# Kernel tuning notes

Hardware: AMD Instinct MI355X
Metric: run time of the kernel (lower is better)

Reference implementation:

```python
import jax, jax.numpy as jnp
import numpy as np

B, T, D = 64, 512, 1024

def setup_inputs() -> dict:
    key = jax.random.key(0)
    k1, k2, k3 = jax.random.split(key, 3)
    q1 = jax.random.normal(k1, (B, T, D), dtype=jnp.float32)
    q2 = jax.random.normal(k2, (B, T, D), dtype=jnp.float32)
    # original uses 'uniform' init; scale like a small uniform weight
    U = jax.random.uniform(k3, (D, D), dtype=jnp.float32, minval=-0.05, maxval=0.05)
    return {"q1": q1, "q2": q2, "U": U}

def reference(q1, q2, U):
    # bilinear scores: (q1 @ U) @ q2^T -> [B, T1, T2]
    att = jnp.einsum('btd,de,bse->bts', q1, U, q2)
    att = jax.nn.relu(att)
    w1_att = jax.nn.softmax(att, axis=1)  # softmax over q1 timesteps
    w2_att = jax.nn.softmax(att, axis=2)  # softmax over q2 timesteps
    # q1_align = w1_att^T @ q1 -> [B, T2, D]
    q1_align = jnp.einsum('bts,btd->bsd', w1_att, q1)
    # q2_align = w2_att @ q2 -> [B, T1, D]
    q2_align = jnp.einsum('bts,bsd->btd', w2_att, q2)
    return (q1_align, q2_align)
```

## Files before the change

kernel.cpp:

```cpp
#include <hip/hip_runtime.h>
#include <hip/hip_bf16.h>
#include <math.h>

#define B_DIM 64
#define T_DIM 512
#define D_DIM 1024
#define TT (T_DIM * T_DIM)
#define TD (T_DIM * D_DIM)
#define PSTR ((long)B_DIM * T_DIM)

typedef _Float16 f16;
typedef f16 f16x4 __attribute__((ext_vector_type(4)));
typedef f16 f16x8 __attribute__((ext_vector_type(8)));
typedef float f32x4 __attribute__((ext_vector_type(4)));

__device__ __forceinline__ void gld_lds16(const void* g, void* l) {
    __builtin_amdgcn_global_load_lds(
        (const __attribute__((address_space(1))) void*)g,
        (__attribute__((address_space(3))) void*)l, 16, 0, 0);
}

#define SWZ(r) (((r) >> 1) & 3)

template <int EPI>
__global__ __launch_bounds__(512, 2) void k_mfma2(
        const f16* __restrict__ A, int lda,
        const f16* __restrict__ Bt, int ldb, int K,
        void* __restrict__ Cout, int ldc,
        const float2* __restrict__ scaleP,
        long batchA, long batchB, long batchC,
        float2* __restrict__ rowP, float2* __restrict__ colP) {
    __shared__ __align__(16) f16 LA[2][8192];
    __shared__ __align__(16) f16 LB[2][8192];

    const int tid = threadIdx.x;
    const int lane = tid & 63, w = tid >> 6;

    const int gX = gridDim.x, gY = gridDim.y;
    int nwg = gX * gY * gridDim.z;
    int o = blockIdx.x + gX * (blockIdx.y + gY * blockIdx.z);
    int q8 = nwg >> 3;
    int fl = (o & 7) * q8 + (o >> 3);
    const int bx = fl % gX;
    int tmp = fl / gX;
    const int by = tmp % gY;
    const int bz = tmp / gY;

    const f16* Ab = A + (long)bz * batchA + (long)(by * 256) * lda;
    const f16* Bb = Bt + (long)bz * batchB + (long)(bx * 256) * ldb;

    const int r0 = tid >> 2, s0 = (tid & 3) ^ SWZ(r0);
    const int r1 = r0 + 128, s1 = (tid & 3) ^ SWZ(r1);
    const long offA0 = (long)r0 * lda + s0 * 8;
    const long offA1 = (long)r1 * lda + s1 * 8;
    const long offB0 = (long)r0 * ldb + s0 * 8;
    const long offB1 = (long)r1 * ldb + s1 * 8;
    const int ldsOff0 = w * 512;
    const int ldsOff1 = 4096 + w * 512;

    const int g = lane >> 4;
    const int rA0 = (w & 1) * 128 + (lane & 15);
    const int rB0 = (w >> 1) * 64 + (lane & 15);

    f32x4 acc[8][4] = {};

    gld_lds16(Ab + offA0, &LA[0][ldsOff0]);
    gld_lds16(Ab + offA1, &LA[0][ldsOff1]);
    gld_lds16(Bb + offB0, &LB[0][ldsOff0]);
    gld_lds16(Bb + offB1, &LB[0][ldsOff1]);
    __syncthreads();

    const int NT = K >> 5;
    for (int t = 0; t < NT; ++t) {
        const int cur = t & 1;
        if (t + 1 < NT) {
            const long kt = (long)(t + 1) << 5;
            gld_lds16(Ab + offA0 + kt, &LA[cur ^ 1][ldsOff0]);
            gld_lds16(Ab + offA1 + kt, &LA[cur ^ 1][ldsOff1]);
            gld_lds16(Bb + offB0 + kt, &LB[cur ^ 1][ldsOff0]);
            gld_lds16(Bb + offB1 + kt, &LB[cur ^ 1][ldsOff1]);
        }
        f16x8 a[8], b[4];
#pragma unroll
        for (int m = 0; m < 8; ++m) {
            int r = rA0 + m * 16;
            a[m] = *(const f16x8*)(&LA[cur][r * 32 + ((g ^ SWZ(r)) << 3)]);
        }
#pragma unroll
        for (int n = 0; n < 4; ++n) {
            int r = rB0 + n * 16;
            b[n] = *(const f16x8*)(&LB[cur][r * 32 + ((g ^ SWZ(r)) << 3)]);
        }
        __builtin_amdgcn_s_setprio(1);
#pragma unroll
        for (int m = 0; m < 8; ++m)
#pragma unroll
            for (int n = 0; n < 4; ++n)
                acc[m][n] = __builtin_amdgcn_mfma_f32_16x16x32_f16(a[m], b[n], acc[m][n], 0, 0, 0);
        __builtin_amdgcn_s_setprio(0);
        __syncthreads();
    }

    const int row0 = by * 256 + (w & 1) * 128 + (lane >> 4) * 4;
    const int col0 = bx * 256 + (w >> 1) * 64 + (lane & 15);

    if constexpr (EPI == 1) {
#pragma unroll
        for (int m = 0; m < 8; ++m)
#pragma unroll
            for (int n = 0; n < 4; ++n)
#pragma unroll
                for (int r = 0; r < 4; ++r)
                    acc[m][n][r] = fmaxf(acc[m][n][r], 0.0f);
        float* C = (float*)Cout + (long)bz * batchC;
#pragma unroll
        for (int m = 0; m < 8; ++m)
#pragma unroll
            for (int r = 0; r < 4; ++r) {
                long row = row0 + m * 16 + r;
#pragma unroll
                for (int n = 0; n < 4; ++n)
                    C[row * ldc + col0 + n * 16] = acc[m][n][r];
            }
        float* redR = (float*)(&LA[0][0]);
        float* redC = redR + 2048;
        const int h = w & 1, cw = w >> 1;
#pragma unroll
        for (int m = 0; m < 8; ++m)
#pragma unroll
            for (int r = 0; r < 4; ++r) {
                float mx = fmaxf(fmaxf(acc[m][0][r], acc[m][1][r]),
                                 fmaxf(acc[m][2][r], acc[m][3][r]));
                mx = fmaxf(mx, __shfl_xor(mx, 1));
                mx = fmaxf(mx, __shfl_xor(mx, 2));
                mx = fmaxf(mx, __shfl_xor(mx, 4));
                mx = fmaxf(mx, __shfl_xor(mx, 8));
                float sm = __expf(acc[m][0][r] - mx) + __expf(acc[m][1][r] - mx)
                         + __expf(acc[m][2][r] - mx) + __expf(acc[m][3][r] - mx);
                sm += __shfl_xor(sm, 1);
                sm += __shfl_xor(sm, 2);
                sm += __shfl_xor(sm, 4);
                sm += __shfl_xor(sm, 8);
                if ((lane & 15) == 0) {
                    int lr = m * 16 + (lane >> 4) * 4 + r;
                    redR[((h * 128 + lr) * 4 + cw) * 2 + 0] = mx;
                    redR[((h * 128 + lr) * 4 + cw) * 2 + 1] = sm;
                }
            }
#pragma unroll
        for (int n = 0; n < 4; ++n) {
            float mx = acc[0][n][0];
#pragma unroll
            for (int m = 0; m < 8; ++m)
#pragma unroll
                for (int r = 0; r < 4; ++r) mx = fmaxf(mx, acc[m][n][r]);
            mx = fmaxf(mx, __shfl_xor(mx, 16));
            mx = fmaxf(mx, __shfl_xor(mx, 32));
            float sm = 0.f;
#pragma unroll
            for (int m = 0; m < 8; ++m)
#pragma unroll
                for (int r = 0; r < 4; ++r) sm += __expf(acc[m][n][r] - mx);
            sm += __shfl_xor(sm, 16);
            sm += __shfl_xor(sm, 32);
            if (lane < 16) {
                int c = cw * 64 + n * 16 + lane;
                redC[(h * 256 + c) * 2 + 0] = mx;
                redC[(h * 256 + c) * 2 + 1] = sm;
            }
        }
        __syncthreads();
        if (tid < 256) {
            float M = -1e30f, S = 0.f;
#pragma unroll
            for (int i = 0; i < 4; ++i) {
                float m_ = redR[(tid * 4 + i) * 2 + 0];
                float s_ = redR[(tid * 4 + i) * 2 + 1];
                float nm = fmaxf(M, m_);
                S = S * __expf(M - nm) + s_ * __expf(m_ - nm);
                M = nm;
            }
            rowP[(long)bx * PSTR + (long)bz * 512 + by * 256 + tid] = make_float2(M, S);
        } else {
            int c = tid - 256;
            float m0_ = redC[c * 2 + 0], s0_ = redC[c * 2 + 1];
            float m1_ = redC[(256 + c) * 2 + 0], s1_ = redC[(256 + c) * 2 + 1];
            float M = fmaxf(m0_, m1_);
            float S = s0_ * __expf(m0_ - M) + s1_ * __expf(m1_ - M);
            colP[(long)by * PSTR + (long)bz * 512 + bx * 256 + c] = make_float2(M, S);
        }
    } else {
        float* C = (float*)Cout + (long)bz * batchC;
        const float2* sp = scaleP + (long)bz * 512;
#pragma unroll
        for (int m = 0; m < 8; ++m)
#pragma unroll
            for (int r = 0; r < 4; ++r) {
                long row = row0 + m * 16 + r;
                float2 pa = sp[row], pb = sp[PSTR + row];
                float M = fmaxf(pa.x, pb.x);
                float S = pa.y * __expf(pa.x - M) + pb.y * __expf(pb.x - M);
                float inv = 1.0f / S;
#pragma unroll
                for (int n = 0; n < 4; ++n)
                    C[row * ldc + col0 + n * 16] = acc[m][n][r] * inv;
            }
    }
}

__global__ __launch_bounds__(256) void k_d1(const float* __restrict__ q1,
                                            f16* __restrict__ q1h, f16* __restrict__ q1ht,
                                            const float* __restrict__ U,
                                            f16* __restrict__ Uht) {
    __shared__ f16 tr[64][72];
    int tid = threadIdx.x;
    int z = blockIdx.z;
    if (z < 64) {
        int b = z;
        int d0 = blockIdx.x * 64, t0 = blockIdx.y * 64;
        const float* S = q1 + ((size_t)b * T_DIM + t0) * D_DIM + d0;
        f16* Dr = q1h + ((size_t)b * T_DIM + t0) * D_DIM + d0;
        int rr = tid >> 4, cc = (tid & 15) * 4;
#pragma unroll
        for (int i = 0; i < 4; ++i) {
            int r = rr + i * 16;
            float4 v = *(const float4*)(S + (size_t)r * D_DIM + cc);
            f16x4 h = {(f16)v.x, (f16)v.y, (f16)v.z, (f16)v.w};
            *(f16x4*)(Dr + (size_t)r * D_DIM + cc) = h;
            tr[cc + 0][r] = h[0];
            tr[cc + 1][r] = h[1];
            tr[cc + 2][r] = h[2];
            tr[cc + 3][r] = h[3];
        }
        __syncthreads();
        f16* Dt = q1ht + ((size_t)b * D_DIM + d0) * T_DIM + t0;
        int r2 = tid >> 3, c8 = (tid & 7) * 8;
#pragma unroll
        for (int i = 0; i < 2; ++i) {
            int d = r2 + i * 32;
            f16x8 vv = *(const f16x8*)(&tr[d][c8]);
            *(f16x8*)(Dt + (size_t)d * T_DIM + c8) = vv;
        }
    } else {
        int pos = blockIdx.y * 16 + blockIdx.x;
        for (int u = 0; u < 2; ++u) {
            int tile = pos + u * 128;
            int n0 = (tile & 15) * 64, k0 = (tile >> 4) * 64;
            int rr = tid >> 4, cc = (tid & 15) * 4;
#pragma unroll
            for (int i = 0; i < 4; ++i) {
                int r = rr + i * 16;
                float4 v = *(const float4*)(U + (size_t)(k0 + r) * D_DIM + n0 + cc);
                tr[cc + 0][r] = (f16)v.x;
                tr[cc + 1][r] = (f16)v.y;
                tr[cc + 2][r] = (f16)v.z;
                tr[cc + 3][r] = (f16)v.w;
            }
            __syncthreads();
            int r2 = tid >> 3, c8 = (tid & 7) * 8;
#pragma unroll
            for (int i = 0; i < 2; ++i) {
                int n = r2 + i * 32;
                f16x8 vv = *(const f16x8*)(&tr[n][c8]);
                *(f16x8*)(Uht + (size_t)(n0 + n) * D_DIM + k0 + c8) = vv;
            }
            __syncthreads();
        }
    }
}

__global__ __launch_bounds__(512, 2) void k_d2(const f16* __restrict__ q1h,
                                               const f16* __restrict__ Uht,
                                               f16* __restrict__ qUh,
                                               const float* __restrict__ q2,
                                               f16* __restrict__ q2h,
                                               f16* __restrict__ q2ht) {
    __shared__ __align__(16) f16 SM[32768];
    int tid = threadIdx.x;
    if (blockIdx.y < 128) {
        f16 (*LA)[8192] = (f16(*)[8192])SM;
        f16 (*LB)[8192] = (f16(*)[8192])(SM + 16384);
        const int lane = tid & 63, w = tid >> 6;
        int o = blockIdx.x + 4 * blockIdx.y;
        int fl = (o & 7) * 64 + (o >> 3);
        int bx = fl & 3, by = fl >> 2;
        const f16* Ab = q1h + (long)(by * 256) * D_DIM;
        const f16* Bb = Uht + (long)(bx * 256) * D_DIM;

        const int r0 = tid >> 2, s0 = (tid & 3) ^ SWZ(r0);
        const int r1 = r0 + 128, s1 = (tid & 3) ^ SWZ(r1);
        const long offA0 = (long)r0 * D_DIM + s0 * 8;
        const long offA1 = (long)r1 * D_DIM + s1 * 8;
        const int ldsOff0 = w * 512, ldsOff1 = 4096 + w * 512;
        const int g = lane >> 4;
        const int rA0 = (w & 1) * 128 + (lane & 15);
        const int rB0 = (w >> 1) * 64 + (lane & 15);

        f32x4 acc[8][4] = {};
        gld_lds16(Ab + offA0, &LA[0][ldsOff0]);
        gld_lds16(Ab + offA1, &LA[0][ldsOff1]);
        gld_lds16(Bb + offA0, &LB[0][ldsOff0]);
        gld_lds16(Bb + offA1, &LB[0][ldsOff1]);
        __syncthreads();

        for (int t = 0; t < 32; ++t) {
            const int cur = t & 1;
            if (t + 1 < 32) {
                const long kt = (long)(t + 1) << 5;
                gld_lds16(Ab + offA0 + kt, &LA[cur ^ 1][ldsOff0]);
                gld_lds16(Ab + offA1 + kt, &LA[cur ^ 1][ldsOff1]);
                gld_lds16(Bb + offA0 + kt, &LB[cur ^ 1][ldsOff0]);
                gld_lds16(Bb + offA1 + kt, &LB[cur ^ 1][ldsOff1]);
            }
            f16x8 a[8], b[4];
#pragma unroll
            for (int m = 0; m < 8; ++m) {
                int r = rA0 + m * 16;
                a[m] = *(const f16x8*)(&LA[cur][r * 32 + ((g ^ SWZ(r)) << 3)]);
            }
#pragma unroll
            for (int n = 0; n < 4; ++n) {
                int r = rB0 + n * 16;
                b[n] = *(const f16x8*)(&LB[cur][r * 32 + ((g ^ SWZ(r)) << 3)]);
            }
            __builtin_amdgcn_s_setprio(1);
#pragma unroll
            for (int m = 0; m < 8; ++m)
#pragma unroll
                for (int n = 0; n < 4; ++n)
                    acc[m][n] = __builtin_amdgcn_mfma_f32_16x16x32_f16(a[m], b[n], acc[m][n], 0, 0, 0);
            __builtin_amdgcn_s_setprio(0);
            __syncthreads();
        }
        const int row0 = by * 256 + (w & 1) * 128 + (lane >> 4) * 4;
        const int col0 = bx * 256 + (w >> 1) * 64 + (lane & 15);
#pragma unroll
        for (int m = 0; m < 8; ++m)
#pragma unroll
            for (int r = 0; r < 4; ++r) {
                long row = row0 + m * 16 + r;
#pragma unroll
                for (int n = 0; n < 4; ++n)
                    qUh[row * D_DIM + col0 + n * 16] = (f16)acc[m][n][r];
            }
    } else {
        int hf = tid >> 8, t2 = tid & 255;
        f16 (*tr)[72] = (f16(*)[72])(SM + hf * 4608);
        int p = (blockIdx.y - 128) * 4 + blockIdx.x;
        int tile = p * 2 + hf;
        int b = tile >> 7, rem = tile & 127;
        int d0 = (rem & 15) * 64, t0 = (rem >> 4) * 64;
        const float* S = q2 + ((size_t)b * T_DIM + t0) * D_DIM + d0;
        f16* Dr = q2h + ((size_t)b * T_DIM + t0) * D_DIM + d0;
        int rr = t2 >> 4, cc = (t2 & 15) * 4;
#pragma unroll
        for (int i = 0; i < 4; ++i) {
            int r = rr + i * 16;
            float4 v = *(const float4*)(S + (size_t)r * D_DIM + cc);
            f16x4 h = {(f16)v.x, (f16)v.y, (f16)v.z, (f16)v.w};
            *(f16x4*)(Dr + (size_t)r * D_DIM + cc) = h;
            tr[cc + 0][r] = h[0];
            tr[cc + 1][r] = h[1];
            tr[cc + 2][r] = h[2];
            tr[cc + 3][r] = h[3];
        }
        __syncthreads();
        f16* Dt = q2ht + ((size_t)b * D_DIM + d0) * T_DIM + t0;
        int r2 = t2 >> 3, c8 = (t2 & 7) * 8;
#pragma unroll
        for (int i = 0; i < 2; ++i) {
            int d = r2 + i * 32;
            f16x8 vv = *(const f16x8*)(&tr[d][c8]);
            *(f16x8*)(Dt + (size_t)d * T_DIM + c8) = vv;
        }
    }
}

__global__ __launch_bounds__(512, 2) void k_d4(const float* __restrict__ att,
                                               const f16* __restrict__ q2ht,
                                               const float2* __restrict__ rowP,
                                               const float2* __restrict__ colP,
                                               float* __restrict__ out2,
                                               f16* __restrict__ P1h) {
    __shared__ __align__(16) f16 SM[33280];
    int tid = threadIdx.x;
    int z = blockIdx.z;
    if (z < 64) {
        f16 (*LA)[8192] = (f16(*)[8192])SM;
        f16 (*LB)[8192] = (f16(*)[8192])(SM + 16384);
        float* rmS = (float*)(SM + 32768);
        const int lane = tid & 63, w = tid >> 6;
        int o = blockIdx.x + 4 * blockIdx.y + 8 * z;
        int fl = (o & 7) * 64 + (o >> 3);
        int bx = fl & 3, by = (fl >> 2) & 1, zb = fl >> 3;

        const float* Abase = att + (long)zb * TT + (long)(by * 256) * T_DIM;
        const f16* Bb = q2ht + (long)zb * TD + (long)(bx * 256) * T_DIM;

        if (tid < 256) {
            float2 pa = rowP[(long)zb * 512 + by * 256 + tid];
            float2 pb = rowP[PSTR + (long)zb * 512 + by * 256 + tid];
            rmS[tid] = fmaxf(pa.x, pb.x);
        }

        const int r0 = tid >> 2, j0 = tid & 3;
        const int r1 = r0 + 128;
        const int sb0 = j0 ^ SWZ(r0), sb1 = j0 ^ SWZ(r1);
        const long offB0 = (long)r0 * T_DIM + sb0 * 8;
        const long offB1 = (long)r1 * T_DIM + sb1 * 8;
        const int ldsOff0 = w * 512, ldsOff1 = 4096 + w * 512;
        const int wA0 = r0 * 32 + ((j0 ^ SWZ(r0)) << 3);
        const int wA1 = r1 * 32 + ((j0 ^ SWZ(r1)) << 3);
        const long srcA0 = (long)r0 * T_DIM + j0 * 8;
        const long srcA1 = (long)r1 * T_DIM + j0 * 8;

        const int g = lane >> 4;
        const int rA0 = (w & 1) * 128 + (lane & 15);
        const int rB0 = (w >> 1) * 64 + (lane & 15);

        __syncthreads();
        const float m0 = rmS[r0], m1 = rmS[r1];

        f32x4 acc[8][4] = {};
        {
            float4 v0 = *(const float4*)(Abase + srcA0);
            float4 v1 = *(const float4*)(Abase + srcA0 + 4);
            float4 v2 = *(const float4*)(Abase + srcA1);
            float4 v3 = *(const float4*)(Abase + srcA1 + 4);
            f16x8 h0 = {(f16)__expf(v0.x - m0), (f16)__expf(v0.y - m0),
                        (f16)__expf(v0.z - m0), (f16)__expf(v0.w - m0),
                        (f16)__expf(v1.x - m0), (f16)__expf(v1.y - m0),
                        (f16)__expf(v1.z - m0), (f16)__expf(v1.w - m0)};
            f16x8 h1 = {(f16)__expf(v2.x - m1), (f16)__expf(v2.y - m1),
                        (f16)__expf(v2.z - m1), (f16)__expf(v2.w - m1),
                        (f16)__expf(v3.x - m1), (f16)__expf(v3.y - m1),
                        (f16)__expf(v3.z - m1), (f16)__expf(v3.w - m1)};
            *(f16x8*)(&LA[0][wA0]) = h0;
            *(f16x8*)(&LA[0][wA1]) = h1;
            gld_lds16(Bb + offB0, &LB[0][ldsOff0]);
            gld_lds16(Bb + offB1, &LB[0][ldsOff1]);
        }
        __syncthreads();

        for (int t = 0; t < 16; ++t) {
            const int cur = t & 1;
            float4 v0, v1, v2, v3;
            if (t + 1 < 16) {
                const long kc = (long)(t + 1) << 5;
                v0 = *(const float4*)(Abase + srcA0 + kc);
                v1 = *(const float4*)(Abase + srcA0 + kc + 4);
                v2 = *(const float4*)(Abase + srcA1 + kc);
                v3 = *(const float4*)(Abase + srcA1 + kc + 4);
                gld_lds16(Bb + offB0 + kc, &LB[cur ^ 1][ldsOff0]);
                gld_lds16(Bb + offB1 + kc, &LB[cur ^ 1][ldsOff1]);
            }
            f16x8 a[8], b[4];
#pragma unroll
            for (int m = 0; m < 8; ++m) {
                int r = rA0 + m * 16;
                a[m] = *(const f16x8*)(&LA[cur][r * 32 + ((g ^ SWZ(r)) << 3)]);
            }
#pragma unroll
            for (int n = 0; n < 4; ++n) {
                int r = rB0 + n * 16;
                b[n] = *(const f16x8*)(&LB[cur][r * 32 + ((g ^ SWZ(r)) << 3)]);
            }
            __builtin_amdgcn_s_setprio(1);
#pragma unroll
            for (int m = 0; m < 8; ++m)
#pragma unroll
                for (int n = 0; n < 4; ++n)
                    acc[m][n] = __builtin_amdgcn_mfma_f32_16x16x32_f16(a[m], b[n], acc[m][n], 0, 0, 0);
            __builtin_amdgcn_s_setprio(0);
            if (t + 1 < 16) {
                f16x8 h0 = {(f16)__expf(v0.x - m0), (f16)__expf(v0.y - m0),
                            (f16)__expf(v0.z - m0), (f16)__expf(v0.w - m0),
                            (f16)__expf(v1.x - m0), (f16)__expf(v1.y - m0),
                            (f16)__expf(v1.z - m0), (f16)__expf(v1.w - m0)};
                f16x8 h1 = {(f16)__expf(v2.x - m1), (f16)__expf(v2.y - m1),
                            (f16)__expf(v2.z - m1), (f16)__expf(v2.w - m1),
                            (f16)__expf(v3.x - m1), (f16)__expf(v3.y - m1),
                            (f16)__expf(v3.z - m1), (f16)__expf(v3.w - m1)};
                *(f16x8*)(&LA[cur ^ 1][wA0]) = h0;
                *(f16x8*)(&LA[cur ^ 1][wA1]) = h1;
            }
            __syncthreads();
        }

        const int row0 = by * 256 + (w & 1) * 128 + (lane >> 4) * 4;
        const int col0 = bx * 256 + (w >> 1) * 64 + (lane & 15);
        float* C = out2 + (long)zb * TD;
        const float2* sp = rowP + (long)zb * 512;
#pragma unroll
        for (int m = 0; m < 8; ++m)
#pragma unroll
            for (int r = 0; r < 4; ++r) {
                long row = row0 + m * 16 + r;
                float2 pa = sp[row], pb = sp[PSTR + row];
                float M = fmaxf(pa.x, pb.x);
                float S = pa.y * __expf(pa.x - M) + pb.y * __expf(pb.x - M);
                float inv = 1.0f / S;
#pragma unroll
                for (int n = 0; n < 4; ++n)
                    C[row * D_DIM + col0 + n * 16] = acc[m][n][r] * inv;
            }
    } else {
        f16 (*tr)[72] = (f16(*)[72])SM;
        float* cmS = (float*)(SM + 16384);
        int id = (z - 64) * 8 + blockIdx.y * 4 + blockIdx.x;
        int b = id >> 6, rem = id & 63;
        int t0 = (rem >> 3) * 64, s0 = (rem & 7) * 64;
        if (tid < 64) {
            float2 pa = colP[(long)b * 512 + s0 + tid];
            float2 pb = colP[PSTR + (long)b * 512 + s0 + tid];
            cmS[tid] = fmaxf(pa.x, pb.x);
        }
        __syncthreads();
        const float* S = att + (long)b * TT + (long)t0 * T_DIM + s0;
        int rr = tid >> 4, cc = (tid & 15) * 4;
#pragma unroll
        for (int i = 0; i < 2; ++i) {
            int r = rr + i * 32;
            float4 v = *(const float4*)(S + (long)r * T_DIM + cc);
            tr[cc + 0][r] = (f16)__expf(v.x - cmS[cc + 0]);
            tr[cc + 1][r] = (f16)__expf(v.y - cmS[cc + 1]);
            tr[cc + 2][r] = (f16)__expf(v.z - cmS[cc + 2]);
            tr[cc + 3][r] = (f16)__expf(v.w - cmS[cc + 3]);
        }
        __syncthreads();
        f16* Dt = P1h + (long)b * TT + (long)s0 * T_DIM + t0;
        int r2 = tid >> 3, c8 = (tid & 7) * 8;
        f16x8 vv = *(const f16x8*)(&tr[r2][c8]);
        *(f16x8*)(Dt + (long)r2 * T_DIM + c8) = vv;
    }
}

extern "C" void kernel_launch(void* const* d_in, const int* in_sizes, int n_in,
                              void* d_out, int out_size, void* d_ws, size_t ws_size,
                              hipStream_t stream) {
    const float* q1 = (const float*)d_in[0];
    const float* q2 = (const float*)d_in[1];
    const float* U  = (const float*)d_in[2];
    float* out = (float*)d_out;

    const size_t BTD = (size_t)B_DIM * TD;
    const size_t DD  = (size_t)D_DIM * D_DIM;
    const size_t BTT = (size_t)B_DIM * TT;

    const size_t need = (5 * BTD + DD) * 2
                      + BTT * 4
                      + BTT * 2
                      + 4 * (size_t)PSTR * sizeof(float2);
    if (need > ws_size) return;

    f16* q1h  = (f16*)d_ws;
    f16* q1ht = q1h  + BTD;
    f16* q2h  = q1ht + BTD;
    f16* q2ht = q2h  + BTD;
    f16* Uht  = q2ht + BTD;
    f16* qUh  = Uht  + DD;
    float* att = (float*)(qUh + BTD);
    f16* P1h  = (f16*)(att + BTT);
    float2* rowP = (float2*)(P1h + BTT);
    float2* colP = rowP + 2 * (size_t)PSTR;

    k_d1<<<dim3(16, 8, 65), 256, 0, stream>>>(q1, q1h, q1ht, U, Uht);
    k_d2<<<dim3(4, 128 + 1024, 1), 512, 0, stream>>>(q1h, Uht, qUh, q2, q2h, q2ht);
    k_mfma2<1><<<dim3(2, 2, 64), 512, 0, stream>>>(
        qUh, D_DIM, q2h, D_DIM, D_DIM, att, T_DIM,
        nullptr, (long)TD, (long)TD, (long)TT, rowP, colP);
    k_d4<<<dim3(4, 2, 64 + 512), 512, 0, stream>>>(
        att, q2ht, rowP, colP, out + BTD, P1h);
    k_mfma2<2><<<dim3(4, 2, 64), 512, 0, stream>>>(
        P1h, T_DIM, q1ht, T_DIM, T_DIM, out, D_DIM,
        colP, (long)TT, (long)TD, (long)TD, nullptr, nullptr);
}
```

Measured before the change: 422.0 us.

## Fuse score exponentials into attention GEMM and merge both alignment GEMMs

The fp32 attention matrix is no longer written and re-read. The score GEMM kernel now emits fp16 exponentiated tiles for the row and column softmax directly, together with partial max/sum statistics. A single alignment kernel then runs both output GEMMs, rescaling the A operand on load with per-tile correction factors. The fp16 copy of q1 is also dropped, and q1 is converted from fp32 inside the qU GEMM's load path. This cuts global memory traffic and kernel launches, but adds extra fp16 rounding of locally-maxed exponentials and register-staged A loads in place of the async LDS copies.

Measured after the change: 387.6 us. -8.2%, faster.

```diff
diff --git a/kernel.cpp b/kernel.cpp
--- a/kernel.cpp
+++ b/kernel.cpp
@@ -22,194 +22,8 @@
 
 #define SWZ(r) (((r) >> 1) & 3)
 
-template <int EPI>
-__global__ __launch_bounds__(512, 2) void k_mfma2(
-        const f16* __restrict__ A, int lda,
-        const f16* __restrict__ Bt, int ldb, int K,
-        void* __restrict__ Cout, int ldc,
-        const float2* __restrict__ scaleP,
-        long batchA, long batchB, long batchC,
-        float2* __restrict__ rowP, float2* __restrict__ colP) {
-    __shared__ __align__(16) f16 LA[2][8192];
-    __shared__ __align__(16) f16 LB[2][8192];
-
-    const int tid = threadIdx.x;
-    const int lane = tid & 63, w = tid >> 6;
-
-    const int gX = gridDim.x, gY = gridDim.y;
-    int nwg = gX * gY * gridDim.z;
-    int o = blockIdx.x + gX * (blockIdx.y + gY * blockIdx.z);
-    int q8 = nwg >> 3;
-    int fl = (o & 7) * q8 + (o >> 3);
-    const int bx = fl % gX;
-    int tmp = fl / gX;
-    const int by = tmp % gY;
-    const int bz = tmp / gY;
-
-    const f16* Ab = A + (long)bz * batchA + (long)(by * 256) * lda;
-    const f16* Bb = Bt + (long)bz * batchB + (long)(bx * 256) * ldb;
-
-    const int r0 = tid >> 2, s0 = (tid & 3) ^ SWZ(r0);
-    const int r1 = r0 + 128, s1 = (tid & 3) ^ SWZ(r1);
-    const long offA0 = (long)r0 * lda + s0 * 8;
-    const long offA1 = (long)r1 * lda + s1 * 8;
-    const long offB0 = (long)r0 * ldb + s0 * 8;
-    const long offB1 = (long)r1 * ldb + s1 * 8;
-    const int ldsOff0 = w * 512;
-    const int ldsOff1 = 4096 + w * 512;
-
-    const int g = lane >> 4;
-    const int rA0 = (w & 1) * 128 + (lane & 15);
-    const int rB0 = (w >> 1) * 64 + (lane & 15);
-
-    f32x4 acc[8][4] = {};
-
-    gld_lds16(Ab + offA0, &LA[0][ldsOff0]);
-    gld_lds16(Ab + offA1, &LA[0][ldsOff1]);
-    gld_lds16(Bb + offB0, &LB[0][ldsOff0]);
-    gld_lds16(Bb + offB1, &LB[0][ldsOff1]);
-    __syncthreads();
-
-    const int NT = K >> 5;
-    for (int t = 0; t < NT; ++t) {
-        const int cur = t & 1;
-        if (t + 1 < NT) {
-            const long kt = (long)(t + 1) << 5;
-            gld_lds16(Ab + offA0 + kt, &LA[cur ^ 1][ldsOff0]);
-            gld_lds16(Ab + offA1 + kt, &LA[cur ^ 1][ldsOff1]);
-            gld_lds16(Bb + offB0 + kt, &LB[cur ^ 1][ldsOff0]);
-            gld_lds16(Bb + offB1 + kt, &LB[cur ^ 1][ldsOff1]);
-        }
-        f16x8 a[8], b[4];
-#pragma unroll
-        for (int m = 0; m < 8; ++m) {
-            int r = rA0 + m * 16;
-            a[m] = *(const f16x8*)(&LA[cur][r * 32 + ((g ^ SWZ(r)) << 3)]);
-        }
-#pragma unroll
-        for (int n = 0; n < 4; ++n) {
-            int r = rB0 + n * 16;
-            b[n] = *(const f16x8*)(&LB[cur][r * 32 + ((g ^ SWZ(r)) << 3)]);
-        }
-        __builtin_amdgcn_s_setprio(1);
-#pragma unroll
-        for (int m = 0; m < 8; ++m)
-#pragma unroll
-            for (int n = 0; n < 4; ++n)
-                acc[m][n] = __builtin_amdgcn_mfma_f32_16x16x32_f16(a[m], b[n], acc[m][n], 0, 0, 0);
-        __builtin_amdgcn_s_setprio(0);
-        __syncthreads();
-    }
-
-    const int row0 = by * 256 + (w & 1) * 128 + (lane >> 4) * 4;
-    const int col0 = bx * 256 + (w >> 1) * 64 + (lane & 15);
-
-    if constexpr (EPI == 1) {
-#pragma unroll
-        for (int m = 0; m < 8; ++m)
-#pragma unroll
-            for (int n = 0; n < 4; ++n)
-#pragma unroll
-                for (int r = 0; r < 4; ++r)
-                    acc[m][n][r] = fmaxf(acc[m][n][r], 0.0f);
-        float* C = (float*)Cout + (long)bz * batchC;
-#pragma unroll
-        for (int m = 0; m < 8; ++m)
-#pragma unroll
-            for (int r = 0; r < 4; ++r) {
-                long row = row0 + m * 16 + r;
-#pragma unroll
-                for (int n = 0; n < 4; ++n)
-                    C[row * ldc + col0 + n * 16] = acc[m][n][r];
-            }
-        float* redR = (float*)(&LA[0][0]);
-        float* redC = redR + 2048;
-        const int h = w & 1, cw = w >> 1;
-#pragma unroll
-        for (int m = 0; m < 8; ++m)
-#pragma unroll
-            for (int r = 0; r < 4; ++r) {
-                float mx = fmaxf(fmaxf(acc[m][0][r], acc[m][1][r]),
-                                 fmaxf(acc[m][2][r], acc[m][3][r]));
-                mx = fmaxf(mx, __shfl_xor(mx, 1));
-                mx = fmaxf(mx, __shfl_xor(mx, 2));
-                mx = fmaxf(mx, __shfl_xor(mx, 4));
-                mx = fmaxf(mx, __shfl_xor(mx, 8));
-                float sm = __expf(acc[m][0][r] - mx) + __expf(acc[m][1][r] - mx)
-                         + __expf(acc[m][2][r] - mx) + __expf(acc[m][3][r] - mx);
-                sm += __shfl_xor(sm, 1);
-                sm += __shfl_xor(sm, 2);
-                sm += __shfl_xor(sm, 4);
-                sm += __shfl_xor(sm, 8);
-                if ((lane & 15) == 0) {
-                    int lr = m * 16 + (lane >> 4) * 4 + r;
-                    redR[((h * 128 + lr) * 4 + cw) * 2 + 0] = mx;
-                    redR[((h * 128 + lr) * 4 + cw) * 2 + 1] = sm;
-                }
-            }
-#pragma unroll
-        for (int n = 0; n < 4; ++n) {
-            float mx = acc[0][n][0];
-#pragma unroll
-            for (int m = 0; m < 8; ++m)
-#pragma unroll
-                for (int r = 0; r < 4; ++r) mx = fmaxf(mx, acc[m][n][r]);
-            mx = fmaxf(mx, __shfl_xor(mx, 16));
-            mx = fmaxf(mx, __shfl_xor(mx, 32));
-            float sm = 0.f;
-#pragma unroll
-            for (int m = 0; m < 8; ++m)
-#pragma unroll
-                for (int r = 0; r < 4; ++r) sm += __expf(acc[m][n][r] - mx);
-            sm += __shfl_xor(sm, 16);
-            sm += __shfl_xor(sm, 32);
-            if (lane < 16) {
-                int c = cw * 64 + n * 16 + lane;
-                redC[(h * 256 + c) * 2 + 0] = mx;
-                redC[(h * 256 + c) * 2 + 1] = sm;
-            }
-        }
-        __syncthreads();
-        if (tid < 256) {
-            float M = -1e30f, S = 0.f;
-#pragma unroll
-            for (int i = 0; i < 4; ++i) {
-                float m_ = redR[(tid * 4 + i) * 2 + 0];
-                float s_ = redR[(tid * 4 + i) * 2 + 1];
-                float nm = fmaxf(M, m_);
-                S = S * __expf(M - nm) + s_ * __expf(m_ - nm);
-                M = nm;
-            }
-            rowP[(long)bx * PSTR + (long)bz * 512 + by * 256 + tid] = make_float2(M, S);
-        } else {
-            int c = tid - 256;
-            float m0_ = redC[c * 2 + 0], s0_ = redC[c * 2 + 1];
-            float m1_ = redC[(256 + c) * 2 + 0], s1_ = redC[(256 + c) * 2 + 1];
-            float M = fmaxf(m0_, m1_);
-            float S = s0_ * __expf(m0_ - M) + s1_ * __expf(m1_ - M);
-            colP[(long)by * PSTR + (long)bz * 512 + bx * 256 + c] = make_float2(M, S);
-        }
-    } else {
-        float* C = (float*)Cout + (long)bz * batchC;
-        const float2* sp = scaleP + (long)bz * 512;
-#pragma unroll
-        for (int m = 0; m < 8; ++m)
-#pragma unroll
-            for (int r = 0; r < 4; ++r) {
-                long row = row0 + m * 16 + r;
-                float2 pa = sp[row], pb = sp[PSTR + row];
-                float M = fmaxf(pa.x, pb.x);
-                float S = pa.y * __expf(pa.x - M) + pb.y * __expf(pb.x - M);
-                float inv = 1.0f / S;
-#pragma unroll
-                for (int n = 0; n < 4; ++n)
-                    C[row * ldc + col0 + n * 16] = acc[m][n][r] * inv;
-            }
-    }
-}
-
 __global__ __launch_bounds__(256) void k_d1(const float* __restrict__ q1,
-                                            f16* __restrict__ q1h, f16* __restrict__ q1ht,
+                                            f16* __restrict__ q1ht,
                                             const float* __restrict__ U,
                                             f16* __restrict__ Uht) {
     __shared__ f16 tr[64][72];
@@ -219,18 +33,15 @@
         int b = z;
         int d0 = blockIdx.x * 64, t0 = blockIdx.y * 64;
         const float* S = q1 + ((size_t)b * T_DIM + t0) * D_DIM + d0;
-        f16* Dr = q1h + ((size_t)b * T_DIM + t0) * D_DIM + d0;
         int rr = tid >> 4, cc = (tid & 15) * 4;
 #pragma unroll
         for (int i = 0; i < 4; ++i) {
             int r = rr + i * 16;
             float4 v = *(const float4*)(S + (size_t)r * D_DIM + cc);
-            f16x4 h = {(f16)v.x, (f16)v.y, (f16)v.z, (f16)v.w};
-            *(f16x4*)(Dr + (size_t)r * D_DIM + cc) = h;
-            tr[cc + 0][r] = h[0];
-            tr[cc + 1][r] = h[1];
-            tr[cc + 2][r] = h[2];
-            tr[cc + 3][r] = h[3];
+            tr[cc + 0][r] = (f16)v.x;
+            tr[cc + 1][r] = (f16)v.y;
+            tr[cc + 2][r] = (f16)v.z;
+            tr[cc + 3][r] = (f16)v.w;
         }
         __syncthreads();
         f16* Dt = q1ht + ((size_t)b * D_DIM + d0) * T_DIM + t0;
@@ -269,7 +80,7 @@
     }
 }
 
-__global__ __launch_bounds__(512, 2) void k_d2(const f16* __restrict__ q1h,
+__global__ __launch_bounds__(512, 2) void k_d2(const float* __restrict__ q1,
                                                const f16* __restrict__ Uht,
                                                f16* __restrict__ qUh,
                                                const float* __restrict__ q2,
@@ -284,33 +95,50 @@
         int o = blockIdx.x + 4 * blockIdx.y;
         int fl = (o & 7) * 64 + (o >> 3);
         int bx = fl & 3, by = fl >> 2;
-        const f16* Ab = q1h + (long)(by * 256) * D_DIM;
+        const float* Aq = q1 + (long)(by * 256) * D_DIM;
         const f16* Bb = Uht + (long)(bx * 256) * D_DIM;
 
-        const int r0 = tid >> 2, s0 = (tid & 3) ^ SWZ(r0);
-        const int r1 = r0 + 128, s1 = (tid & 3) ^ SWZ(r1);
-        const long offA0 = (long)r0 * D_DIM + s0 * 8;
-        const long offA1 = (long)r1 * D_DIM + s1 * 8;
+        const int r0 = tid >> 2, j0 = tid & 3;
+        const int r1 = r0 + 128;
+        const long srcA0 = (long)r0 * D_DIM + j0 * 8;
+        const long srcA1 = (long)r1 * D_DIM + j0 * 8;
+        const int wA0 = r0 * 32 + ((j0 ^ SWZ(r0)) << 3);
+        const int wA1 = r1 * 32 + ((j0 ^ SWZ(r1)) << 3);
+        const long offB0 = (long)r0 * D_DIM + (j0 ^ SWZ(r0)) * 8;
+        const long offB1 = (long)r1 * D_DIM + (j0 ^ SWZ(r1)) * 8;
         const int ldsOff0 = w * 512, ldsOff1 = 4096 + w * 512;
         const int g = lane >> 4;
         const int rA0 = (w & 1) * 128 + (lane & 15);
         const int rB0 = (w >> 1) * 64 + (lane & 15);
 
         f32x4 acc[8][4] = {};
-        gld_lds16(Ab + offA0, &LA[0][ldsOff0]);
-        gld_lds16(Ab + offA1, &LA[0][ldsOff1]);
-        gld_lds16(Bb + offA0, &LB[0][ldsOff0]);
-        gld_lds16(Bb + offA1, &LB[0][ldsOff1]);
+        {
+            float4 v0 = *(const float4*)(Aq + srcA0);
+            float4 v1 = *(const float4*)(Aq + srcA0 + 4);
+            float4 v2 = *(const float4*)(Aq + srcA1);
+            float4 v3 = *(const float4*)(Aq + srcA1 + 4);
+            f16x8 h0 = {(f16)v0.x, (f16)v0.y, (f16)v0.z, (f16)v0.w,
+                        (f16)v1.x, (f16)v1.y, (f16)v1.z, (f16)v1.w};
+            f16x8 h1 = {(f16)v2.x, (f16)v2.y, (f16)v2.z, (f16)v2.w,
+                        (f16)v3.x, (f16)v3.y, (f16)v3.z, (f16)v3.w};
+            *(f16x8*)(&LA[0][wA0]) = h0;
+            *(f16x8*)(&LA[0][wA1]) = h1;
+            gld_lds16(Bb + offB0, &LB[0][ldsOff0]);
+            gld_lds16(Bb + offB1, &LB[0][ldsOff1]);
+        }
         __syncthreads();
 
         for (int t = 0; t < 32; ++t) {
             const int cur = t & 1;
+            float4 v0, v1, v2, v3;
             if (t + 1 < 32) {
-                const long kt = (long)(t + 1) << 5;
-                gld_lds16(Ab + offA0 + kt, &LA[cur ^ 1][ldsOff0]);
-                gld_lds16(Ab + offA1 + kt, &LA[cur ^ 1][ldsOff1]);
-                gld_lds16(Bb + offA0 + kt, &LB[cur ^ 1][ldsOff0]);
-                gld_lds16(Bb + offA1 + kt, &LB[cur ^ 1][ldsOff1]);
+                const long kc = (long)(t + 1) << 5;
+                v0 = *(const float4*)(Aq + srcA0 + kc);
+                v1 = *(const float4*)(Aq + srcA0 + kc + 4);
+                v2 = *(const float4*)(Aq + srcA1 + kc);
+                v3 = *(const float4*)(Aq + srcA1 + kc + 4);
+                gld_lds16(Bb + offB0 + kc, &LB[cur ^ 1][ldsOff0]);
+                gld_lds16(Bb + offB1 + kc, &LB[cur ^ 1][ldsOff1]);
             }
             f16x8 a[8], b[4];
 #pragma unroll
@@ -330,6 +158,14 @@
                 for (int n = 0; n < 4; ++n)
                     acc[m][n] = __builtin_amdgcn_mfma_f32_16x16x32_f16(a[m], b[n], acc[m][n], 0, 0, 0);
             __builtin_amdgcn_s_setprio(0);
+            if (t + 1 < 32) {
+                f16x8 h0 = {(f16)v0.x, (f16)v0.y, (f16)v0.z, (f16)v0.w,
+                            (f16)v1.x, (f16)v1.y, (f16)v1.z, (f16)v1.w};
+                f16x8 h1 = {(f16)v2.x, (f16)v2.y, (f16)v2.z, (f16)v2.w,
+                            (f16)v3.x, (f16)v3.y, (f16)v3.z, (f16)v3.w};
+                *(f16x8*)(&LA[cur ^ 1][wA0]) = h0;
+                *(f16x8*)(&LA[cur ^ 1][wA1]) = h1;
+            }
             __syncthreads();
         }
         const int row0 = by * 256 + (w & 1) * 128 + (lane >> 4) * 4;
@@ -376,163 +212,291 @@
     }
 }
 
-__global__ __launch_bounds__(512, 2) void k_d4(const float* __restrict__ att,
-                                               const f16* __restrict__ q2ht,
-                                               const float2* __restrict__ rowP,
-                                               const float2* __restrict__ colP,
-                                               float* __restrict__ out2,
-                                               f16* __restrict__ P1h) {
-    __shared__ __align__(16) f16 SM[33280];
-    int tid = threadIdx.x;
-    int z = blockIdx.z;
-    if (z < 64) {
-        f16 (*LA)[8192] = (f16(*)[8192])SM;
-        f16 (*LB)[8192] = (f16(*)[8192])(SM + 16384);
-        float* rmS = (float*)(SM + 32768);
-        const int lane = tid & 63, w = tid >> 6;
-        int o = blockIdx.x + 4 * blockIdx.y + 8 * z;
-        int fl = (o & 7) * 64 + (o >> 3);
-        int bx = fl & 3, by = (fl >> 2) & 1, zb = fl >> 3;
-
-        const float* Abase = att + (long)zb * TT + (long)(by * 256) * T_DIM;
-        const f16* Bb = q2ht + (long)zb * TD + (long)(bx * 256) * T_DIM;
-
-        if (tid < 256) {
-            float2 pa = rowP[(long)zb * 512 + by * 256 + tid];
-            float2 pb = rowP[PSTR + (long)zb * 512 + by * 256 + tid];
-            rmS[tid] = fmaxf(pa.x, pb.x);
-        }
-
-        const int r0 = tid >> 2, j0 = tid & 3;
-        const int r1 = r0 + 128;
-        const int sb0 = j0 ^ SWZ(r0), sb1 = j0 ^ SWZ(r1);
-        const long offB0 = (long)r0 * T_DIM + sb0 * 8;
-        const long offB1 = (long)r1 * T_DIM + sb1 * 8;
-        const int ldsOff0 = w * 512, ldsOff1 = 4096 + w * 512;
-        const int wA0 = r0 * 32 + ((j0 ^ SWZ(r0)) << 3);
-        const int wA1 = r1 * 32 + ((j0 ^ SWZ(r1)) << 3);
-        const long srcA0 = (long)r0 * T_DIM + j0 * 8;
-        const long srcA1 = (long)r1 * T_DIM + j0 * 8;
-
-        const int g = lane >> 4;
-        const int rA0 = (w & 1) * 128 + (lane & 15);
-        const int rB0 = (w >> 1) * 64 + (lane & 15);
-
+__global__ __launch_bounds__(512, 2) void k_att3(const f16* __restrict__ qUh,
+                                                 const f16* __restrict__ q2h,
+                                                 f16* __restrict__ P2,
+                                                 f16* __restrict__ P1,
+                                                 float2* __restrict__ rowP,
+                                                 float2* __restrict__ colP) {
+    __shared__ __align__(16) f16 LA[2][8192];
+    __shared__ __align__(16) f16 LB[2][8192];
+    const int tid = threadIdx.x;
+    const int lane = tid & 63, w = tid >> 6;
+
+    int o = blockIdx.x + 2 * (blockIdx.y + 2 * blockIdx.z);
+    int fl = (o & 7) * 32 + (o >> 3);
+    const int bx = fl & 1, by = (fl >> 1) & 1, zb = fl >> 2;
+
+    const f16* Ab = qUh + (long)(zb * 512 + by * 256) * D_DIM;
+    const f16* Bb = q2h + (long)zb * TD + (long)(bx * 256) * D_DIM;
+
+    const int r0 = tid >> 2, j0 = tid & 3;
+    const int r1 = r0 + 128;
+    const long offA0 = (long)r0 * D_DIM + (j0 ^ SWZ(r0)) * 8;
+    const long offA1 = (long)r1 * D_DIM + (j0 ^ SWZ(r1)) * 8;
+    const int ldsOff0 = w * 512, ldsOff1 = 4096 + w * 512;
+    const int g = lane >> 4;
+    const int rA0 = (w & 1) * 128 + (lane & 15);
+    const int rB0 = (w >> 1) * 64 + (lane & 15);
+
+    f32x4 acc[8][4] = {};
+
+    gld_lds16(Ab + offA0, &LA[0][ldsOff0]);
+    gld_lds16(Ab + offA1, &LA[0][ldsOff1]);
+    gld_lds16(Bb + offA0, &LB[0][ldsOff0]);
+    gld_lds16(Bb + offA1, &LB[0][ldsOff1]);
+    __syncthreads();
+
+    for (int t = 0; t < 32; ++t) {
+        const int cur = t & 1;
+        if (t + 1 < 32) {
+            const long kt = (long)(t + 1) << 5;
+            gld_lds16(Ab + offA0 + kt, &LA[cur ^ 1][ldsOff0]);
+            gld_lds16(Ab + offA1 + kt, &LA[cur ^ 1][ldsOff1]);
+            gld_lds16(Bb + offA0 + kt, &LB[cur ^ 1][ldsOff0]);
+            gld_lds16(Bb + offA1 + kt, &LB[cur ^ 1][ldsOff1]);
+        }
+        f16x8 a[8], b[4];
+#pragma unroll
+        for (int m = 0; m < 8; ++m) {
+            int r = rA0 + m * 16;
+            a[m] = *(const f16x8*)(&LA[cur][r * 32 + ((g ^ SWZ(r)) << 3)]);
+        }
+#pragma unroll
+        for (int n = 0; n < 4; ++n) {
+            int r = rB0 + n * 16;
+            b[n] = *(const f16x8*)(&LB[cur][r * 32 + ((g ^ SWZ(r)) << 3)]);
+        }
+        __builtin_amdgcn_s_setprio(1);
+#pragma unroll
+        for (int m = 0; m < 8; ++m)
+#pragma unroll
+            for (int n = 0; n < 4; ++n)
+                acc[m][n] = __builtin_amdgcn_mfma_f32_16x16x32_f16(a[m], b[n], acc[m][n], 0, 0, 0);
+        __builtin_amdgcn_s_setprio(0);
         __syncthreads();
-        const float m0 = rmS[r0], m1 = rmS[r1];
-
-        f32x4 acc[8][4] = {};
-        {
-            float4 v0 = *(const float4*)(Abase + srcA0);
-            float4 v1 = *(const float4*)(Abase + srcA0 + 4);
-            float4 v2 = *(const float4*)(Abase + srcA1);
-            float4 v3 = *(const float4*)(Abase + srcA1 + 4);
-            f16x8 h0 = {(f16)__expf(v0.x - m0), (f16)__expf(v0.y - m0),
-                        (f16)__expf(v0.z - m0), (f16)__expf(v0.w - m0),
-                        (f16)__expf(v1.x - m0), (f16)__expf(v1.y - m0),
-                        (f16)__expf(v1.z - m0), (f16)__expf(v1.w - m0)};
-            f16x8 h1 = {(f16)__expf(v2.x - m1), (f16)__expf(v2.y - m1),
-                        (f16)__expf(v2.z - m1), (f16)__expf(v2.w - m1),
-                        (f16)__expf(v3.x - m1), (f16)__expf(v3.y - m1),
-                        (f16)__expf(v3.z - m1), (f16)__expf(v3.w - m1)};
-            *(f16x8*)(&LA[0][wA0]) = h0;
-            *(f16x8*)(&LA[0][wA1]) = h1;
-            gld_lds16(Bb + offB0, &LB[0][ldsOff0]);
-            gld_lds16(Bb + offB1, &LB[0][ldsOff1]);
+    }
+
+#pragma unroll
+    for (int m = 0; m < 8; ++m)
+#pragma unroll
+        for (int n = 0; n < 4; ++n)
+#pragma unroll
+            for (int r = 0; r < 4; ++r)
+                acc[m][n][r] = fmaxf(acc[m][n][r], 0.0f);
+
+    float* redR = (float*)(&LA[0][0]);
+    float* redC = redR + 2048;
+    float* rowM = redC + 1024;
+    float* colM = rowM + 256;
+    const int h = w & 1, cw = w >> 1;
+#pragma unroll
+    for (int m = 0; m < 8; ++m)
+#pragma unroll
+        for (int r = 0; r < 4; ++r) {
+            float mx = fmaxf(fmaxf(acc[m][0][r], acc[m][1][r]),
+                             fmaxf(acc[m][2][r], acc[m][3][r]));
+            mx = fmaxf(mx, __shfl_xor(mx, 1));
+            mx = fmaxf(mx, __shfl_xor(mx, 2));
+            mx = fmaxf(mx, __shfl_xor(mx, 4));
+            mx = fmaxf(mx, __shfl_xor(mx, 8));
+            float sm = __expf(acc[m][0][r] - mx) + __expf(acc[m][1][r] - mx)
+                     + __expf(acc[m][2][r] - mx) + __expf(acc[m][3][r] - mx);
+            sm += __shfl_xor(sm, 1);
+            sm += __shfl_xor(sm, 2);
+            sm += __shfl_xor(sm, 4);
+            sm += __shfl_xor(sm, 8);
+            if ((lane & 15) == 0) {
+                int lr = m * 16 + (lane >> 4) * 4 + r;
+                redR[((h * 128 + lr) * 4 + cw) * 2 + 0] = mx;
+                redR[((h * 128 + lr) * 4 + cw) * 2 + 1] = sm;
+            }
+        }
+#pragma unroll
+    for (int n = 0; n < 4; ++n) {
+        float mx = acc[0][n][0];
+#pragma unroll
+        for (int m = 0; m < 8; ++m)
+#pragma unroll
+            for (int r = 0; r < 4; ++r) mx = fmaxf(mx, acc[m][n][r]);
+        mx = fmaxf(mx, __shfl_xor(mx, 16));
+        mx = fmaxf(mx, __shfl_xor(mx, 32));
+        float sm = 0.f;
+#pragma unroll
+        for (int m = 0; m < 8; ++m)
+#pragma unroll
+            for (int r = 0; r < 4; ++r) sm += __expf(acc[m][n][r] - mx);
+        sm += __shfl_xor(sm, 16);
+        sm += __shfl_xor(sm, 32);
+        if (lane < 16) {
+            int c = cw * 64 + n * 16 + lane;
+            redC[(h * 256 + c) * 2 + 0] = mx;
+            redC[(h * 256 + c) * 2 + 1] = sm;
+        }
+    }
+    __syncthreads();
+    if (tid < 256) {
+        float M = -1e30f, S = 0.f;
+#pragma unroll
+        for (int i = 0; i < 4; ++i) {
+            float m_ = redR[(tid * 4 + i) * 2 + 0];
+            float s_ = redR[(tid * 4 + i) * 2 + 1];
+            float nm = fmaxf(M, m_);
+            S = S * __expf(M - nm) + s_ * __expf(m_ - nm);
+            M = nm;
+        }
+        rowP[(long)bx * PSTR + (long)zb * 512 + by * 256 + tid] = make_float2(M, S);
+        rowM[tid] = M;
+    } else {
+        int c = tid - 256;
+        float m0_ = redC[c * 2 + 0], s0_ = redC[c * 2 + 1];
+        float m1_ = redC[(256 + c) * 2 + 0], s1_ = redC[(256 + c) * 2 + 1];
+        float M = fmaxf(m0_, m1_);
+        float S = s0_ * __expf(m0_ - M) + s1_ * __expf(m1_ - M);
+        colP[(long)by * PSTR + (long)zb * 512 + bx * 256 + c] = make_float2(M, S);
+        colM[c] = M;
+    }
+    __syncthreads();
+
+    f16* P2b = P2 + (long)zb * TT;
+#pragma unroll
+    for (int m = 0; m < 8; ++m)
+#pragma unroll
+        for (int r = 0; r < 4; ++r) {
+            int Lr = h * 128 + m * 16 + (lane >> 4) * 4 + r;
+            float M = rowM[Lr];
+            long base = (long)(by * 256 + Lr) * T_DIM + bx * 256;
+#pragma unroll
+            for (int n = 0; n < 4; ++n) {
+                int c = cw * 64 + n * 16 + (lane & 15);
+                P2b[base + c] = (f16)__expf(acc[m][n][r] - M);
+            }
+        }
+    f16* P1b = P1 + (long)zb * TT;
+#pragma unroll
+    for (int m = 0; m < 8; ++m) {
+        int Lt = h * 128 + m * 16 + (lane >> 4) * 4;
+#pragma unroll
+        for (int n = 0; n < 4; ++n) {
+            int Lc = cw * 64 + n * 16 + (lane & 15);
+            float M = colM[Lc];
+            f16x4 v = {(f16)__expf(acc[m][n][0] - M), (f16)__expf(acc[m][n][1] - M),
+                       (f16)__expf(acc[m][n][2] - M), (f16)__expf(acc[m][n][3] - M)};
+            *(f16x4*)(&P1b[(long)(bx * 256 + Lc) * T_DIM + by * 256 + Lt]) = v;
+        }
+    }
+}
+
+__global__ __launch_bounds__(512, 2) void k_align(
+        const f16* __restrict__ P2, const f16* __restrict__ q2ht,
+        const float2* __restrict__ rowP, float* __restrict__ outQ2,
+        const f16* __restrict__ P1, const f16* __restrict__ q1ht,
+        const float2* __restrict__ colP, float* __restrict__ outQ1) {
+    __shared__ __align__(16) f16 LA[2][8192];
+    __shared__ __align__(16) f16 LB[2][8192];
+    const int tid = threadIdx.x;
+    const int lane = tid & 63, w = tid >> 6;
+
+    int o = blockIdx.x + 4 * (blockIdx.y + 2 * blockIdx.z);
+    int fl = (o & 7) * 128 + (o >> 3);
+    const int bx = fl & 3, by = (fl >> 2) & 1, z = fl >> 3;
+    const int zb = z & 63;
+
+    const f16* P  = (z < 64) ? P2 : P1;
+    const f16* Bt = (z < 64) ? q2ht : q1ht;
+    const float2* sp = ((z < 64) ? rowP : colP) + (long)zb * 512;
+    float* out = ((z < 64) ? outQ2 : outQ1) + (long)zb * TD;
+
+    const f16* Ab = P + (long)zb * TT + (long)(by * 256) * T_DIM;
+    const f16* Bb = Bt + (long)zb * TD + (long)(bx * 256) * T_DIM;
+
+    const int r0 = tid >> 2, j0 = tid & 3;
+    const int r1 = r0 + 128;
+    float2 pa0 = sp[by * 256 + r0], pb0 = sp[PSTR + by * 256 + r0];
+    float M0 = fmaxf(pa0.x, pb0.x);
+    f16 f00 = (f16)__expf(pa0.x - M0), f01 = (f16)__expf(pb0.x - M0);
+    float2 pa1 = sp[by * 256 + r1], pb1 = sp[PSTR + by * 256 + r1];
+    float M1 = fmaxf(pa1.x, pb1.x);
+    f16 f10 = (f16)__expf(pa1.x - M1), f11 = (f16)__expf(pb1.x - M1);
+
+    const long srcA0 = (long)r0 * T_DIM + j0 * 8;
+    const long srcA1 = (long)r1 * T_DIM + j0 * 8;
+    const int wA0 = r0 * 32 + ((j0 ^ SWZ(r0)) << 3);
+    const int wA1 = r1 * 32 + ((j0 ^ SWZ(r1)) << 3);
+    const long offB0 = (long)r0 * T_DIM + (j0 ^ SWZ(r0)) * 8;
+    const long offB1 = (long)r1 * T_DIM + (j0 ^ SWZ(r1)) * 8;
+    const int ldsOff0 = w * 512, ldsOff1 = 4096 + w * 512;
+    const int g = lane >> 4;
+    const int rA0 = (w & 1) * 128 + (lane & 15);
+    const int rB0 = (w >> 1) * 64 + (lane & 15);
+
+    f32x4 acc[8][4] = {};
+    {
+        f16x8 a0 = *(const f16x8*)(Ab + srcA0);
+        f16x8 a1 = *(const f16x8*)(Ab + srcA1);
+#pragma unroll
+        for (int i = 0; i < 8; ++i) { a0[i] *= f00; a1[i] *= f10; }
+        *(f16x8*)(&LA[0][wA0]) = a0;
+        *(f16x8*)(&LA[0][wA1]) = a1;
+        gld_lds16(Bb + offB0, &LB[0][ldsOff0]);
+        gld_lds16(Bb + offB1, &LB[0][ldsOff1]);
+    }
+    __syncthreads();
+
+    for (int t = 0; t < 16; ++t) {
+        const int cur = t & 1;
+        f16x8 a0n, a1n;
+        if (t + 1 < 16) {
+            const long kc = (long)(t + 1) << 5;
+            a0n = *(const f16x8*)(Ab + srcA0 + kc);
+            a1n = *(const f16x8*)(Ab + srcA1 + kc);
+            gld_lds16(Bb + offB0 + kc, &LB[cur ^ 1][ldsOff0]);
+            gld_lds16(Bb + offB1 + kc, &LB[cur ^ 1][ldsOff1]);
+        }
+        f16x8 a[8], b[4];
+#pragma unroll
+        for (int m = 0; m < 8; ++m) {
+            int r = rA0 + m * 16;
+            a[m] = *(const f16x8*)(&LA[cur][r * 32 + ((g ^ SWZ(r)) << 3)]);
+        }
+#pragma unroll
+        for (int n = 0; n < 4; ++n) {
+            int r = rB0 + n * 16;
+            b[n] = *(const f16x8*)(&LB[cur][r * 32 + ((g ^ SWZ(r)) << 3)]);
+        }
+        __builtin_amdgcn_s_setprio(1);
+#pragma unroll
+        for (int m = 0; m < 8; ++m)
+#pragma unroll
+            for (int n = 0; n < 4; ++n)
+                acc[m][n] = __builtin_amdgcn_mfma_f32_16x16x32_f16(a[m], b[n], acc[m][n], 0, 0, 0);
+        __builtin_amdgcn_s_setprio(0);
+        if (t + 1 < 16) {
+            f16 fa = ((t + 1) & 8) ? f01 : f00;
+            f16 fb = ((t + 1) & 8) ? f11 : f10;
+#pragma unroll
+            for (int i = 0; i < 8; ++i) { a0n[i] *= fa; a1n[i] *= fb; }
+            *(f16x8*)(&LA[cur ^ 1][wA0]) = a0n;
+            *(f16x8*)(&LA[cur ^ 1][wA1]) = a1n;
         }
         __syncthreads();
-
-        for (int t = 0; t < 16; ++t) {
-            const int cur = t & 1;
-            float4 v0, v1, v2, v3;
-            if (t + 1 < 16) {
-                const long kc = (long)(t + 1) << 5;
-                v0 = *(const float4*)(Abase + srcA0 + kc);
-                v1 = *(const float4*)(Abase + srcA0 + kc + 4);
-                v2 = *(const float4*)(Abase + srcA1 + kc);
-                v3 = *(const float4*)(Abase + srcA1 + kc + 4);
-                gld_lds16(Bb + offB0 + kc, &LB[cur ^ 1][ldsOff0]);
-                gld_lds16(Bb + offB1 + kc, &LB[cur ^ 1][ldsOff1]);
-            }
-            f16x8 a[8], b[4];
-#pragma unroll
-            for (int m = 0; m < 8; ++m) {
-                int r = rA0 + m * 16;
-                a[m] = *(const f16x8*)(&LA[cur][r * 32 + ((g ^ SWZ(r)) << 3)]);
-            }
-#pragma unroll
-            for (int n = 0; n < 4; ++n) {
-                int r = rB0 + n * 16;
-                b[n] = *(const f16x8*)(&LB[cur][r * 32 + ((g ^ SWZ(r)) << 3)]);
-            }
-            __builtin_amdgcn_s_setprio(1);
-#pragma unroll
-            for (int m = 0; m < 8; ++m)
-#pragma unroll
-                for (int n = 0; n < 4; ++n)
-                    acc[m][n] = __builtin_amdgcn_mfma_f32_16x16x32_f16(a[m], b[n], acc[m][n], 0, 0, 0);
-            __builtin_amdgcn_s_setprio(0);
-            if (t + 1 < 16) {
-                f16x8 h0 = {(f16)__expf(v0.x - m0), (f16)__expf(v0.y - m0),
-                            (f16)__expf(v0.z - m0), (f16)__expf(v0.w - m0),
-                            (f16)__expf(v1.x - m0), (f16)__expf(v1.y - m0),
-                            (f16)__expf(v1.z - m0), (f16)__expf(v1.w - m0)};
-                f16x8 h1 = {(f16)__expf(v2.x - m1), (f16)__expf(v2.y - m1),
-                            (f16)__expf(v2.z - m1), (f16)__expf(v2.w - m1),
-                            (f16)__expf(v3.x - m1), (f16)__expf(v3.y - m1),
-                            (f16)__expf(v3.z - m1), (f16)__expf(v3.w - m1)};
-                *(f16x8*)(&LA[cur ^ 1][wA0]) = h0;
-                *(f16x8*)(&LA[cur ^ 1][wA1]) = h1;
-            }
-            __syncthreads();
-        }
-
-        const int row0 = by * 256 + (w & 1) * 128 + (lane >> 4) * 4;
-        const int col0 = bx * 256 + (w >> 1) * 64 + (lane & 15);
-        float* C = out2 + (long)zb * TD;
-        const float2* sp = rowP + (long)zb * 512;
-#pragma unroll
-        for (int m = 0; m < 8; ++m)
-#pragma unroll
-            for (int r = 0; r < 4; ++r) {
-                long row = row0 + m * 16 + r;
-                float2 pa = sp[row], pb = sp[PSTR + row];
-                float M = fmaxf(pa.x, pb.x);
-                float S = pa.y * __expf(pa.x - M) + pb.y * __expf(pb.x - M);
-                float inv = 1.0f / S;
-#pragma unroll
-                for (int n = 0; n < 4; ++n)
-                    C[row * D_DIM + col0 + n * 16] = acc[m][n][r] * inv;
-            }
-    } else {
-        f16 (*tr)[72] = (f16(*)[72])SM;
-        float* cmS = (float*)(SM + 16384);
-        int id = (z - 64) * 8 + blockIdx.y * 4 + blockIdx.x;
-        int b = id >> 6, rem = id & 63;
-        int t0 = (rem >> 3) * 64, s0 = (rem & 7) * 64;
-        if (tid < 64) {
-            float2 pa = colP[(long)b * 512 + s0 + tid];
-            float2 pb = colP[PSTR + (long)b * 512 + s0 + tid];
-            cmS[tid] = fmaxf(pa.x, pb.x);
-        }
-        __syncthreads();
-        const float* S = att + (long)b * TT + (long)t0 * T_DIM + s0;
-        int rr = tid >> 4, cc = (tid & 15) * 4;
-#pragma unroll
-        for (int i = 0; i < 2; ++i) {
-            int r = rr + i * 32;
-            float4 v = *(const float4*)(S + (long)r * T_DIM + cc);
-            tr[cc + 0][r] = (f16)__expf(v.x - cmS[cc + 0]);
-            tr[cc + 1][r] = (f16)__expf(v.y - cmS[cc + 1]);
-            tr[cc + 2][r] = (f16)__expf(v.z - cmS[cc + 2]);
-            tr[cc + 3][r] = (f16)__expf(v.w - cmS[cc + 3]);
-        }
-        __syncthreads();
-        f16* Dt = P1h + (long)b * TT + (long)s0 * T_DIM + t0;
-        int r2 = tid >> 3, c8 = (tid & 7) * 8;
-        f16x8 vv = *(const f16x8*)(&tr[r2][c8]);
-        *(f16x8*)(Dt + (long)r2 * T_DIM + c8) = vv;
-    }
+    }
+
+    const int row0 = by * 256 + (w & 1) * 128 + (lane >> 4) * 4;
+    const int col0 = bx * 256 + (w >> 1) * 64 + (lane & 15);
+#pragma unroll
+    for (int m = 0; m < 8; ++m)
+#pragma unroll
+        for (int r = 0; r < 4; ++r) {
+            int row = row0 + m * 16 + r;
+            float2 pa = sp[row], pb = sp[PSTR + row];
+            float M = fmaxf(pa.x, pb.x);
+            float S = pa.y * __expf(pa.x - M) + pb.y * __expf(pb.x - M);
+            float inv = 1.0f / S;
+#pragma unroll
+            for (int n = 0; n < 4; ++n)
+                out[(long)row * D_DIM + col0 + n * 16] = acc[m][n][r] * inv;
+        }
 }
 
 extern "C" void kernel_launch(void* const* d_in, const int* in_sizes, int n_in,
@@ -547,31 +511,24 @@
     const size_t DD  = (size_t)D_DIM * D_DIM;
     const size_t BTT = (size_t)B_DIM * TT;
 
-    const size_t need = (5 * BTD + DD) * 2
-                      + BTT * 4
-                      + BTT * 2
+    const size_t need = (4 * BTD + DD) * 2
+                      + 2 * BTT * 2
                       + 4 * (size_t)PSTR * sizeof(float2);
     if (need > ws_size) return;
 
-    f16* q1h  = (f16*)d_ws;
-    f16* q1ht = q1h  + BTD;
+    f16* q1ht = (f16*)d_ws;
     f16* q2h  = q1ht + BTD;
     f16* q2ht = q2h  + BTD;
     f16* Uht  = q2ht + BTD;
     f16* qUh  = Uht  + DD;
-    float* att = (float*)(qUh + BTD);
-    f16* P1h  = (f16*)(att + BTT);
-    float2* rowP = (float2*)(P1h + BTT);
+    f16* P2   = qUh  + BTD;
+    f16* P1   = P2   + BTT;
+    float2* rowP = (float2*)(P1 + BTT);
     float2* colP = rowP + 2 * (size_t)PSTR;
 
-    k_d1<<<dim3(16, 8, 65), 256, 0, stream>>>(q1, q1h, q1ht, U, Uht);
-    k_d2<<<dim3(4, 128 + 1024, 1), 512, 0, stream>>>(q1h, Uht, qUh, q2, q2h, q2ht);
-    k_mfma2<1><<<dim3(2, 2, 64), 512, 0, stream>>>(
-        qUh, D_DIM, q2h, D_DIM, D_DIM, att, T_DIM,
-        nullptr, (long)TD, (long)TD, (long)TT, rowP, colP);
-    k_d4<<<dim3(4, 2, 64 + 512), 512, 0, stream>>>(
-        att, q2ht, rowP, colP, out + BTD, P1h);
-    k_mfma2<2><<<dim3(4, 2, 64), 512, 0, stream>>>(
-        P1h, T_DIM, q1ht, T_DIM, T_DIM, out, D_DIM,
-        colP, (long)TT, (long)TD, (long)TD, nullptr, nullptr);
+    k_d1<<<dim3(16, 8, 65), 256, 0, stream>>>(q1, q1ht, U, Uht);
+    k_d2<<<dim3(4, 128 + 1024, 1), 512, 0, stream>>>(q1, Uht, qUh, q2, q2h, q2ht);
+    k_att3<<<dim3(2, 2, 64), 512, 0, stream>>>(qUh, q2h, P2, P1, rowP, colP);
+    k_align<<<dim3(4, 2, 128), 512, 0, stream>>>(
+        P2, q2ht, rowP, out + BTD, P1, q1ht, colP, out);
 }
```
